# Kernel tuning notes

Measured on AMD Instinct MI355X. Metric: run time of the kernel, lower is better.

Reference implementation:

```python
import jax, jax.numpy as jnp
import numpy as np

M, NQ, NKV, DX, DT = 8, 1024, 1024, 512, 2
H, HD = 8, 64            # num_heads, head_dim
INNER = H * HD           # 512
KHID = 16                # kernel MLP hidden dim
SCALE = HD ** -0.5


def setup_inputs() -> dict:
    key = jax.random.key(0)
    ks = jax.random.split(key, 16)
    s = lambda fan_in: 1.0 / np.sqrt(fan_in)
    return {
        "xq": jax.random.normal(ks[0], (M, NQ, DX), jnp.float32),
        "xk": jax.random.normal(ks[1], (M, NKV, DX), jnp.float32),
        "xv": jax.random.normal(ks[2], (M, NKV, DX), jnp.float32),
        "tq": jax.random.normal(ks[3], (M, NQ, DT), jnp.float32),
        "tk": jax.random.normal(ks[4], (M, NKV, DT), jnp.float32),
        # attention projections (bias=False for q/k/v, Linear bias for out)
        "w_q": jax.random.normal(ks[5], (DX, INNER), jnp.float32) * s(DX),
        "w_k": jax.random.normal(ks[6], (DX, INNER), jnp.float32) * s(DX),
        "w_v": jax.random.normal(ks[7], (DX, INNER), jnp.float32) * s(DX),
        "w_out": jax.random.normal(ks[8], (INNER, DX), jnp.float32) * s(INNER),
        "b_out": jnp.zeros((DX,), jnp.float32),
        # kernel MLP: dt -> KHID -> H (per-head pairwise bias)
        "kw1": jax.random.normal(ks[9], (DT, KHID), jnp.float32) * s(DT),
        "kb1": jnp.zeros((KHID,), jnp.float32),
        "kw2": jax.random.normal(ks[10], (KHID, H), jnp.float32) * s(KHID),
        "kb2": jnp.zeros((H,), jnp.float32),
    }


def reference(xq, xk, xv, tq, tk, w_q, w_k, w_v, w_out, b_out, kw1, kb1, kw2, kb2):
    # pairwise differences of input locations: [m, nq, nkv, dt]
    diff = tq[:, :, None, :] - tk[:, None, :, :]
    # kernel MLP -> per-head bias, rearranged to [m, h, nq, nkv]
    hmid = jax.nn.relu(diff @ kw1 + kb1)          # [m, nq, nkv, KHID]
    dots = jnp.einsum('mqkc,ch->mhqk', hmid, kw2) + kb2[None, :, None, None]
    # token attention: standard scaled QK scores
    q = (xq @ w_q).reshape(M, NQ, H, HD)          # [m, nq, h, d]
    k = (xk @ w_k).reshape(M, NKV, H, HD)
    token_dots = jnp.einsum('mqhd,mkhd->mhqk', q, k) * SCALE
    dots = dots + token_dots
    attn = jax.nn.softmax(dots, axis=-1)          # softmax over keys
    v = (xv @ w_v).reshape(M, NKV, H, HD)
    out = jnp.einsum('mhqk,mkhd->mqhd', attn, v).reshape(M, NQ, INNER)
    return out @ w_out + b_out                    # [m, nq, dx]
```

## Files before the change

### kernel.cpp

```cpp
#include <hip/hip_runtime.h>


typedef unsigned short u16;
typedef unsigned int   u32;
typedef short bf8 __attribute__((ext_vector_type(8)));
typedef float f4  __attribute__((ext_vector_type(4)));
typedef _Float16 h2 __attribute__((ext_vector_type(2)));

#define Mb 8
#define LOG2E 1.44269504088896f
#define SCALE2 (0.125f * LOG2E)
#define NTOK 4194304

__device__ __forceinline__ u16 f2bf(float f) {
    union { float f; u32 u; } v; v.f = f;
    u32 r = v.u + 0x7fffu + ((v.u >> 16) & 1u);
    return (u16)(r >> 16);
}
__device__ __forceinline__ u32 pk2(float a, float b) {
    u32 r;
    asm("v_cvt_pk_bf16_f32 %0, %1, %2" : "=v"(r) : "v"(a), "v"(b));
    return r;
}
__device__ __forceinline__ void gl_lds16(const u16* g, u16* l) {
    __builtin_amdgcn_global_load_lds(
        (const __attribute__((address_space(1))) u32*)g,
        (__attribute__((address_space(3))) u32*)l, 16, 0, 0);
}
__device__ __forceinline__ h2 h2_of(u32 x) {
    union { u32 u; h2 h; } c; c.u = x; return c.h;
}
__device__ __forceinline__ u32 u_of(h2 x) {
    union { h2 h; u32 u; } c; c.h = x; return c.u;
}
__device__ __forceinline__ float dot2(h2 a, h2 b, float c) {
#if __has_builtin(__builtin_amdgcn_fdot2)
    return __builtin_amdgcn_fdot2(a, b, c, false);
#else
    return fmaf((float)a[0], (float)b[0], fmaf((float)a[1], (float)b[1], c));
#endif
}

struct PArgs {
    const float* ws[4];
    u16* dstW;
};

__global__ __launch_bounds__(256) void prep(PArgs p) {
    __shared__ u16 tl[64][80];
    const int tid = threadIdx.x;
    const int bb = blockIdx.x;
    const int mat = bb >> 6, t = bb & 63;
    const int kt = t >> 3, nt = t & 7;
    const float* src = p.ws[mat] + (size_t)kt * 64 * 512 + (size_t)nt * 64;
    const int r0 = tid >> 4, c4 = (tid & 15) * 4;
    #pragma unroll
    for (int rr = 0; rr < 4; ++rr) {
        const int row = r0 + rr * 16;
        float4 a = *(const float4*)(src + (size_t)row * 512 + c4);
        tl[c4 + 0][row] = f2bf(a.x);
        tl[c4 + 1][row] = f2bf(a.y);
        tl[c4 + 2][row] = f2bf(a.z);
        tl[c4 + 3][row] = f2bf(a.w);
    }
    __syncthreads();
    u16* dst = p.dstW + (size_t)mat * 262144 + (size_t)nt * 64 * 512 + (size_t)kt * 64;
    #pragma unroll
    for (int i = 0; i < 2; ++i) {
        const int s2 = tid + i * 256;
        const int nrow = s2 >> 3, k8 = (s2 & 7) * 8;
        *(uint4*)(dst + (size_t)nrow * 512 + k8) = *(const uint4*)&tl[nrow][k8];
    }
}

struct GArgs {
    const void*  A[3];
    const u16*   W[3];
    void*        C[3];
    const float* bias;
    int          modeT[3];
    int          outf32;
    int          af32;
};

__global__ __launch_bounds__(256) void gemm_mfma(GArgs g) {
    __shared__ u16 Xs[128][32];
    __shared__ u16 Ws[128][32];

    const int z   = blockIdx.z;
    const int tid = threadIdx.x;
    const int w = tid >> 6, lane = tid & 63, quad = lane >> 4, l16 = lane & 15;
    const int wm = w >> 1, wn = w & 1;
    const int n0 = blockIdx.x * 128, t0 = blockIdx.y * 128;
    const int trans = g.modeT[z];

    f4 acc[4][4];
    #pragma unroll
    for (int i = 0; i < 4; ++i)
        #pragma unroll
        for (int j = 0; j < 4; ++j) acc[i][j] = (f4)0.f;

    const int lrow  = lane >> 2;
    const int kslot = (lane & 3) ^ ((lane >> 3) & 3);
    u16* ldsW0 = &Ws[w * 32][0];
    u16* ldsW1 = &Ws[w * 32 + 16][0];
    const u16* gW0 = g.W[z] + (size_t)(n0 + w * 32 + lrow) * 512 + kslot * 8;
    const u16* gW1 = gW0 + 16 * 512;

    u16* ldsX0 = &Xs[w * 32][0];
    u16* ldsX1 = &Xs[w * 32 + 16][0];
    const u16* gA0 = (const u16*)g.A[z] + (size_t)(t0 + w * 32 + lrow) * 512 + kslot * 8;
    const u16* gA1 = gA0 + 16 * 512;
    const int arow_s = tid >> 1, ah = tid & 1;
    const float* aF = (const float*)g.A[z] + (size_t)(t0 + arow_s) * 512 + ah * 16;
    const int s_sw = (arow_s >> 1) & 3;
    u16* aw0 = &Xs[arow_s][((2 * ah)     ^ s_sw) * 8];
    u16* aw1 = &Xs[arow_s][((2 * ah + 1) ^ s_sw) * 8];

    const int rslot = (quad ^ ((l16 >> 1) & 3)) * 8;

    for (int kc = 0; kc < 512; kc += 32) {
        __syncthreads();
        if (g.af32) {
            float4 f0 = *(const float4*)(aF + kc);
            float4 f1 = *(const float4*)(aF + kc + 4);
            float4 f2 = *(const float4*)(aF + kc + 8);
            float4 f3 = *(const float4*)(aF + kc + 12);
            uint4 v0, v1;
            v0.x = pk2(f0.x, f0.y); v0.y = pk2(f0.z, f0.w);
            v0.z = pk2(f1.x, f1.y); v0.w = pk2(f1.z, f1.w);
            v1.x = pk2(f2.x, f2.y); v1.y = pk2(f2.z, f2.w);
            v1.z = pk2(f3.x, f3.y); v1.w = pk2(f3.z, f3.w);
            *(uint4*)aw0 = v0;
            *(uint4*)aw1 = v1;
        } else {
            gl_lds16(gA0 + kc, ldsX0);
            gl_lds16(gA1 + kc, ldsX1);
        }
        gl_lds16(gW0 + kc, ldsW0);
        gl_lds16(gW1 + kc, ldsW1);
        __syncthreads();

        const u16* Abase = trans ? &Xs[0][0] : &Ws[0][0];
        const u16* Bbase = trans ? &Ws[0][0] : &Xs[0][0];
        const int arow = (trans ? wm : wn) * 64;
        const int brow = (trans ? wn : wm) * 64;
        bf8 af[4], bf[4];
        #pragma unroll
        for (int i = 0; i < 4; ++i)
            af[i] = *(const bf8*)(Abase + (arow + i * 16 + l16) * 32 + rslot);
        #pragma unroll
        for (int j = 0; j < 4; ++j)
            bf[j] = *(const bf8*)(Bbase + (brow + j * 16 + l16) * 32 + rslot);
        #pragma unroll
        for (int i = 0; i < 4; ++i)
            #pragma unroll
            for (int j = 0; j < 4; ++j)
                acc[i][j] = __builtin_amdgcn_mfma_f32_16x16x32_bf16(af[i], bf[j], acc[i][j], 0, 0, 0);
    }

    if (g.outf32) {
        float* Co = (float*)g.C[z];
        #pragma unroll
        for (int i = 0; i < 4; ++i) {
            const int nb = n0 + wn * 64 + i * 16 + quad * 4;
            float4 bv = *(const float4*)&g.bias[nb];
            #pragma unroll
            for (int j = 0; j < 4; ++j) {
                const int tok = t0 + wm * 64 + j * 16 + l16;
                float4 st;
                st.x = acc[i][j][0] + bv.x; st.y = acc[i][j][1] + bv.y;
                st.z = acc[i][j][2] + bv.z; st.w = acc[i][j][3] + bv.w;
                *(float4*)&Co[(size_t)tok * 512 + nb] = st;
            }
        }
    } else if (!trans) {
        u16* C = (u16*)g.C[z];
        #pragma unroll
        for (int i = 0; i < 4; ++i) {
            const int nb = n0 + wn * 64 + i * 16 + quad * 4;
            #pragma unroll
            for (int j = 0; j < 4; ++j) {
                const int tok = t0 + wm * 64 + j * 16 + l16;
                uint2 pw;
                pw.x = pk2(acc[i][j][0], acc[i][j][1]);
                pw.y = pk2(acc[i][j][2], acc[i][j][3]);
                *(uint2*)&C[(size_t)tok * 512 + nb] = pw;
            }
        }
    } else {
        u16* Vt = (u16*)g.C[z];
        #pragma unroll
        for (int i = 0; i < 4; ++i) {
            const int tokb = t0 + wm * 64 + i * 16 + quad * 4;
            const int mb = tokb >> 10, tb = tokb & 1023;
            #pragma unroll
            for (int j = 0; j < 4; ++j) {
                const int n = n0 + wn * 64 + j * 16 + l16;
                uint2 pw;
                pw.x = pk2(acc[i][j][0], acc[i][j][1]);
                pw.y = pk2(acc[i][j][2], acc[i][j][3]);
                *(uint2*)&Vt[(size_t)mb * 524288 + (size_t)n * 1024 + tb] = pw;
            }
        }
    }
}

__global__ __launch_bounds__(512) void attn_mfma(
    const u16* __restrict__ Q, const u16* __restrict__ K,
    const u16* __restrict__ Vt,
    const float* __restrict__ tqp, const float* __restrict__ tkp,
    const float* __restrict__ kw1, const float* __restrict__ kb1,
    const float* __restrict__ kw2,
    u16* __restrict__ O)
{
    __shared__ u16 sK[2][8][64][8];
    __shared__ u16 sV[2][8][64][8];
    __shared__ u32 sv2[2][8][68];
    __shared__ u16 sP[8][16][68];

    const int tid = threadIdx.x;
    const int w = tid >> 6, lane = tid & 63, quad = lane >> 4, l16 = lane & 15;
    const int b = (blockIdx.z * 8 + blockIdx.y) * 8 + blockIdx.x;
    const int xc = b & 7, j = b >> 3;
    const int hm = xc * 8 + (j & 7);
    const int qt = j >> 3;
    const int h = hm & 7, m = hm >> 3;
    const int q0 = qt * 128;
    const size_t qtok = (size_t)m * 1024 + q0 + w * 16 + l16;

    bf8 qf[2];
    {
        const u16* qp = Q + qtok * 512 + h * 64 + quad * 8;
        qf[0] = *(const bf8*)qp;
        qf[1] = *(const bf8*)(qp + 32);
    }
    h2 u2[8], w2p[8];
    {
        const float t0v = tqp[qtok * 2], t1v = tqp[qtok * 2 + 1];
        #pragma unroll
        for (int cp = 0; cp < 8; ++cp) {
            const int c0 = 2 * cp, c1 = 2 * cp + 1;
            float ua = fmaf(t0v, kw1[c0], fmaf(t1v, kw1[16 + c0], kb1[c0]));
            float ub = fmaf(t0v, kw1[c1], fmaf(t1v, kw1[16 + c1], kb1[c1]));
            u2[cp][0]  = (_Float16)ua;  u2[cp][1]  = (_Float16)ub;
            w2p[cp][0] = (_Float16)(LOG2E * kw2[c0 * 8 + h]);
            w2p[cp][1] = (_Float16)(LOG2E * kw2[c1 * 8 + h]);
        }
    }
    const float w0a = kw1[2 * w],     w1a = kw1[16 + 2 * w];
    const float w0b = kw1[2 * w + 1], w1b = kw1[16 + 2 * w + 1];

    const u16* gK = K + ((size_t)m * 1024 + lane) * 512 + h * 64 + w * 8;
    const u16* gV = Vt + (size_t)m * 524288 + (size_t)(h * 64 + lane) * 1024 + w * 8;
    const float* gT = tkp + (size_t)m * 2048 + lane * 2;

    float mrun = -1e30f, lrun = 0.f;
    f4 o[4];
    #pragma unroll
    for (int d = 0; d < 4; ++d) o[d] = (f4)0.f;

    auto STAGE = [&](int kt2, int nb) {
        const int k0n = kt2 * 64;
        float2 t = *(const float2*)(gT + k0n * 2);
        h2 pv;
        pv[0] = (_Float16)fmaf(t.x, w0a, t.y * w1a);
        pv[1] = (_Float16)fmaf(t.x, w0b, t.y * w1b);
        sv2[nb][w][lane] = u_of(pv);
        gl_lds16(gK + (size_t)k0n * 512, &sK[nb][w][0][0]);
        gl_lds16(gV + k0n,               &sV[nb][w][0][0]);
    };

    STAGE(0, 0);
    __syncthreads();

    int cur = 0;
    for (int kt = 0; kt < 16; ++kt) {
        if (kt < 15) STAGE(kt + 1, cur ^ 1);

        f4 s[4];
        #pragma unroll
        for (int msub = 0; msub < 4; ++msub) {
            bf8 kf0 = *(const bf8*)&sK[cur][quad][msub * 16 + l16][0];
            bf8 kf1 = *(const bf8*)&sK[cur][4 + quad][msub * 16 + l16][0];
            s[msub] = __builtin_amdgcn_mfma_f32_16x16x32_bf16(kf0, qf[0], (f4)0.f, 0, 0, 0);
            s[msub] = __builtin_amdgcn_mfma_f32_16x16x32_bf16(kf1, qf[1], s[msub], 0, 0, 0);
        }
        #pragma unroll
        for (int msub = 0; msub < 4; ++msub) {
            const int kb = msub * 16 + quad * 4;
            f4 b2 = (f4)0.f;
            #pragma unroll
            for (int cp = 0; cp < 8; ++cp) {
                uint4 vv = *(const uint4*)&sv2[cur][cp][kb];
                const h2 uc = u2[cp], wc = w2p[cp];
                const h2 z = (h2)(_Float16)0.f;
                h2 d0 = uc - h2_of(vv.x);
                h2 d1 = uc - h2_of(vv.y);
                h2 d2 = uc - h2_of(vv.z);
                h2 d3 = uc - h2_of(vv.w);
                d0 = __builtin_elementwise_max(d0, z);
                d1 = __builtin_elementwise_max(d1, z);
                d2 = __builtin_elementwise_max(d2, z);
                d3 = __builtin_elementwise_max(d3, z);
                b2[0] = dot2(d0, wc, b2[0]);
                b2[1] = dot2(d1, wc, b2[1]);
                b2[2] = dot2(d2, wc, b2[2]);
                b2[3] = dot2(d3, wc, b2[3]);
            }
            s[msub] = s[msub] * SCALE2 + b2;
        }
        float mx = -1e30f;
        #pragma unroll
        for (int msub = 0; msub < 4; ++msub) {
            mx = fmaxf(mx, fmaxf(fmaxf(s[msub][0], s[msub][1]),
                                 fmaxf(s[msub][2], s[msub][3])));
        }
        mx = fmaxf(mx, __shfl_xor(mx, 16));
        mx = fmaxf(mx, __shfl_xor(mx, 32));
        const float mnew = fmaxf(mrun, mx);
        float ps = 0.f;
        #pragma unroll
        for (int msub = 0; msub < 4; ++msub) {
            #pragma unroll
            for (int r = 0; r < 4; ++r) {
                float p = exp2f(s[msub][r] - mnew);
                s[msub][r] = p;
                ps += p;
            }
        }
        ps += __shfl_xor(ps, 16);
        ps += __shfl_xor(ps, 32);
        if (__all(mx <= mrun)) {
            lrun += ps;
        } else {
            const float alpha = exp2f(mrun - mnew);
            lrun = lrun * alpha + ps;
            mrun = mnew;
            #pragma unroll
            for (int d = 0; d < 4; ++d) o[d] = o[d] * alpha;
        }
        #pragma unroll
        for (int msub = 0; msub < 4; ++msub) {
            uint2 pw;
            pw.x = pk2(s[msub][0], s[msub][1]);
            pw.y = pk2(s[msub][2], s[msub][3]);
            *(uint2*)&sP[w][l16][msub * 16 + quad * 4] = pw;
        }
        #pragma unroll
        for (int dsub = 0; dsub < 4; ++dsub) {
            #pragma unroll
            for (int kc2 = 0; kc2 < 2; ++kc2) {
                bf8 vf = *(const bf8*)&sV[cur][kc2 * 4 + quad][dsub * 16 + l16][0];
                bf8 pf = *(const bf8*)&sP[w][l16][kc2 * 32 + quad * 8];
                o[dsub] = __builtin_amdgcn_mfma_f32_16x16x32_bf16(vf, pf, o[dsub], 0, 0, 0);
            }
        }

        if (kt < 15) __syncthreads();
        cur ^= 1;
    }

    const float inv = 1.f / lrun;
    #pragma unroll
    for (int dsub = 0; dsub < 4; ++dsub) {
        uint2 pw;
        pw.x = pk2(o[dsub][0] * inv, o[dsub][1] * inv);
        pw.y = pk2(o[dsub][2] * inv, o[dsub][3] * inv);
        *(uint2*)&O[qtok * 512 + h * 64 + dsub * 16 + quad * 4] = pw;
    }
}

extern "C" void kernel_launch(void* const* d_in, const int* in_sizes, int n_in,
                              void* d_out, int out_size, void* d_ws, size_t ws_size,
                              hipStream_t stream) {
    const float* xq    = (const float*)d_in[0];
    const float* xk    = (const float*)d_in[1];
    const float* xv    = (const float*)d_in[2];
    const float* tq    = (const float*)d_in[3];
    const float* tk    = (const float*)d_in[4];
    const float* w_q   = (const float*)d_in[5];
    const float* w_k   = (const float*)d_in[6];
    const float* w_v   = (const float*)d_in[7];
    const float* w_out = (const float*)d_in[8];
    const float* b_out = (const float*)d_in[9];
    const float* kw1   = (const float*)d_in[10];
    const float* kb1   = (const float*)d_in[11];
    const float* kw2   = (const float*)d_in[12];

    u16* Q  = (u16*)d_ws;
    u16* Kp = Q  + NTOK;
    u16* Vt = Kp + NTOK;
    u16* O  = Vt + NTOK;
    u16* Wq = O  + 3 * (size_t)NTOK;
    u16* Wk = Wq + 262144;
    u16* Wv = Wk + 262144;
    u16* Wo = Wv + 262144;

    PArgs p;
    p.ws[0] = w_q; p.ws[1] = w_k; p.ws[2] = w_v; p.ws[3] = w_out;
    p.dstW = Wq;
    prep<<<dim3(256), 256, 0, stream>>>(p);

    GArgs gq;
    gq.A[0] = xq;  gq.A[1] = xk;  gq.A[2] = xv;
    gq.W[0] = Wq;  gq.W[1] = Wk;  gq.W[2] = Wv;
    gq.C[0] = Q;   gq.C[1] = Kp;  gq.C[2] = Vt;
    gq.bias = nullptr;
    gq.modeT[0] = 0; gq.modeT[1] = 0; gq.modeT[2] = 1;
    gq.outf32 = 0; gq.af32 = 1;
    gemm_mfma<<<dim3(4, 64, 3), 256, 0, stream>>>(gq);

    attn_mfma<<<dim3(8, 8, Mb), 512, 0, stream>>>(Q, Kp, Vt, tq, tk,
                                                  kw1, kb1, kw2, O);

    GArgs go;
    go.A[0] = O;   go.A[1] = O;   go.A[2] = O;
    go.W[0] = Wo;  go.W[1] = Wo;  go.W[2] = Wo;
    go.C[0] = d_out; go.C[1] = d_out; go.C[2] = d_out;
    go.bias = b_out;
    go.modeT[0] = 0; go.modeT[1] = 0; go.modeT[2] = 0;
    go.outf32 = 1; go.af32 = 0;
    gemm_mfma<<<dim3(4, 64, 1), 256, 0, stream>>>(go);
}
```

Measured before the change: 259.7 us.

## Fuse output projection into attention epilogue via per-head atomic accumulation

Removes the separate output-projection GEMM and its bf16 O intermediate. Each attention wave now multiplies its normalized head output by the matching slice of W_out with MFMA and atomically adds the partial result into the fp32 output. The prep kernel pre-fills the output with the bias, and the gemm kernel drops its unused fp32-output and bf16-A paths. It trades a kernel launch and an O round-trip for many scattered, non-coalesced float atomics (eight heads per output element). It also replaces exp2 with the LOG2E folded into the weights by __expf, which adds a multiply per element.

After: 616.0 us. +137.2%, slower.

```diff
diff --git a/kernel.cpp b/kernel.cpp
--- a/kernel.cpp
+++ b/kernel.cpp
@@ -8,8 +8,7 @@
 typedef _Float16 h2 __attribute__((ext_vector_type(2)));
 
 #define Mb 8
-#define LOG2E 1.44269504088896f
-#define SCALE2 (0.125f * LOG2E)
+#define SCALE 0.125f
 #define NTOK 4194304
 
 __device__ __forceinline__ u16 f2bf(float f) {
@@ -44,32 +43,45 @@
 struct PArgs {
     const float* ws[4];
     u16* dstW;
+    const float* bias;
+    float* outp;
 };
 
 __global__ __launch_bounds__(256) void prep(PArgs p) {
     __shared__ u16 tl[64][80];
     const int tid = threadIdx.x;
-    const int bb = blockIdx.x;
-    const int mat = bb >> 6, t = bb & 63;
-    const int kt = t >> 3, nt = t & 7;
-    const float* src = p.ws[mat] + (size_t)kt * 64 * 512 + (size_t)nt * 64;
-    const int r0 = tid >> 4, c4 = (tid & 15) * 4;
-    #pragma unroll
-    for (int rr = 0; rr < 4; ++rr) {
-        const int row = r0 + rr * 16;
-        float4 a = *(const float4*)(src + (size_t)row * 512 + c4);
-        tl[c4 + 0][row] = f2bf(a.x);
-        tl[c4 + 1][row] = f2bf(a.y);
-        tl[c4 + 2][row] = f2bf(a.z);
-        tl[c4 + 3][row] = f2bf(a.w);
-    }
-    __syncthreads();
-    u16* dst = p.dstW + (size_t)mat * 262144 + (size_t)nt * 64 * 512 + (size_t)kt * 64;
-    #pragma unroll
-    for (int i = 0; i < 2; ++i) {
-        const int s2 = tid + i * 256;
-        const int nrow = s2 >> 3, k8 = (s2 & 7) * 8;
-        *(uint4*)(dst + (size_t)nrow * 512 + k8) = *(const uint4*)&tl[nrow][k8];
+    const int b = blockIdx.x;
+    if (b < 256) {
+        const int mat = b >> 6, t = b & 63;
+        const int kt = t >> 3, nt = t & 7;
+        const float* src = p.ws[mat] + (size_t)kt * 64 * 512 + (size_t)nt * 64;
+        const int r0 = tid >> 4, c4 = (tid & 15) * 4;
+        #pragma unroll
+        for (int rr = 0; rr < 4; ++rr) {
+            const int row = r0 + rr * 16;
+            float4 a = *(const float4*)(src + (size_t)row * 512 + c4);
+            tl[c4 + 0][row] = f2bf(a.x);
+            tl[c4 + 1][row] = f2bf(a.y);
+            tl[c4 + 2][row] = f2bf(a.z);
+            tl[c4 + 3][row] = f2bf(a.w);
+        }
+        __syncthreads();
+        u16* dst = p.dstW + (size_t)mat * 262144 + (size_t)nt * 64 * 512 + (size_t)kt * 64;
+        #pragma unroll
+        for (int i = 0; i < 2; ++i) {
+            const int s2 = tid + i * 256;
+            const int nrow = s2 >> 3, k8 = (s2 & 7) * 8;
+            *(uint4*)(dst + (size_t)nrow * 512 + k8) = *(const uint4*)&tl[nrow][k8];
+        }
+    } else {
+        const int bb = b - 256;
+        const int tok = bb * 16 + (tid >> 4);
+        const int c0 = (tid & 15) * 8;
+        float* dst = p.outp + (size_t)tok * 512;
+        const float4* bsrc = (const float4*)p.bias;
+        #pragma unroll
+        for (int i = 0; i < 8; ++i)
+            *(float4*)(dst + (c0 + i) * 4) = bsrc[c0 + i];
     }
 }
 
@@ -77,10 +89,7 @@
     const void*  A[3];
     const u16*   W[3];
     void*        C[3];
-    const float* bias;
     int          modeT[3];
-    int          outf32;
-    int          af32;
 };
 
 __global__ __launch_bounds__(256) void gemm_mfma(GArgs g) {
@@ -107,10 +116,6 @@
     const u16* gW0 = g.W[z] + (size_t)(n0 + w * 32 + lrow) * 512 + kslot * 8;
     const u16* gW1 = gW0 + 16 * 512;
 
-    u16* ldsX0 = &Xs[w * 32][0];
-    u16* ldsX1 = &Xs[w * 32 + 16][0];
-    const u16* gA0 = (const u16*)g.A[z] + (size_t)(t0 + w * 32 + lrow) * 512 + kslot * 8;
-    const u16* gA1 = gA0 + 16 * 512;
     const int arow_s = tid >> 1, ah = tid & 1;
     const float* aF = (const float*)g.A[z] + (size_t)(t0 + arow_s) * 512 + ah * 16;
     const int s_sw = (arow_s >> 1) & 3;
@@ -121,7 +126,7 @@
 
     for (int kc = 0; kc < 512; kc += 32) {
         __syncthreads();
-        if (g.af32) {
+        {
             float4 f0 = *(const float4*)(aF + kc);
             float4 f1 = *(const float4*)(aF + kc + 4);
             float4 f2 = *(const float4*)(aF + kc + 8);
@@ -133,9 +138,6 @@
             v1.z = pk2(f3.x, f3.y); v1.w = pk2(f3.z, f3.w);
             *(uint4*)aw0 = v0;
             *(uint4*)aw1 = v1;
-        } else {
-            gl_lds16(gA0 + kc, ldsX0);
-            gl_lds16(gA1 + kc, ldsX1);
         }
         gl_lds16(gW0 + kc, ldsW0);
         gl_lds16(gW1 + kc, ldsW1);
@@ -159,22 +161,7 @@
                 acc[i][j] = __builtin_amdgcn_mfma_f32_16x16x32_bf16(af[i], bf[j], acc[i][j], 0, 0, 0);
     }
 
-    if (g.outf32) {
-        float* Co = (float*)g.C[z];
-        #pragma unroll
-        for (int i = 0; i < 4; ++i) {
-            const int nb = n0 + wn * 64 + i * 16 + quad * 4;
-            float4 bv = *(const float4*)&g.bias[nb];
-            #pragma unroll
-            for (int j = 0; j < 4; ++j) {
-                const int tok = t0 + wm * 64 + j * 16 + l16;
-                float4 st;
-                st.x = acc[i][j][0] + bv.x; st.y = acc[i][j][1] + bv.y;
-                st.z = acc[i][j][2] + bv.z; st.w = acc[i][j][3] + bv.w;
-                *(float4*)&Co[(size_t)tok * 512 + nb] = st;
-            }
-        }
-    } else if (!trans) {
+    if (!trans) {
         u16* C = (u16*)g.C[z];
         #pragma unroll
         for (int i = 0; i < 4; ++i) {
@@ -212,7 +199,7 @@
     const float* __restrict__ tqp, const float* __restrict__ tkp,
     const float* __restrict__ kw1, const float* __restrict__ kb1,
     const float* __restrict__ kw2,
-    u16* __restrict__ O)
+    const u16* __restrict__ Wo, float* __restrict__ Oout)
 {
     __shared__ u16 sK[2][8][64][8];
     __shared__ u16 sV[2][8][64][8];
@@ -243,9 +230,8 @@
             const int c0 = 2 * cp, c1 = 2 * cp + 1;
             float ua = fmaf(t0v, kw1[c0], fmaf(t1v, kw1[16 + c0], kb1[c0]));
             float ub = fmaf(t0v, kw1[c1], fmaf(t1v, kw1[16 + c1], kb1[c1]));
-            u2[cp][0]  = (_Float16)ua;  u2[cp][1]  = (_Float16)ub;
-            w2p[cp][0] = (_Float16)(LOG2E * kw2[c0 * 8 + h]);
-            w2p[cp][1] = (_Float16)(LOG2E * kw2[c1 * 8 + h]);
+            u2[cp][0]  = (_Float16)ua;              u2[cp][1]  = (_Float16)ub;
+            w2p[cp][0] = (_Float16)kw2[c0 * 8 + h]; w2p[cp][1] = (_Float16)kw2[c1 * 8 + h];
         }
     }
     const float w0a = kw1[2 * w],     w1a = kw1[16 + 2 * w];
@@ -308,7 +294,7 @@
                 b2[2] = dot2(d2, wc, b2[2]);
                 b2[3] = dot2(d3, wc, b2[3]);
             }
-            s[msub] = s[msub] * SCALE2 + b2;
+            s[msub] = s[msub] * SCALE + b2;
         }
         float mx = -1e30f;
         #pragma unroll
@@ -324,7 +310,7 @@
         for (int msub = 0; msub < 4; ++msub) {
             #pragma unroll
             for (int r = 0; r < 4; ++r) {
-                float p = exp2f(s[msub][r] - mnew);
+                float p = __expf(s[msub][r] - mnew);
                 s[msub][r] = p;
                 ps += p;
             }
@@ -334,7 +320,7 @@
         if (__all(mx <= mrun)) {
             lrun += ps;
         } else {
-            const float alpha = exp2f(mrun - mnew);
+            const float alpha = __expf(mrun - mnew);
             lrun = lrun * alpha + ps;
             mrun = mnew;
             #pragma unroll
@@ -367,7 +353,23 @@
         uint2 pw;
         pw.x = pk2(o[dsub][0] * inv, o[dsub][1] * inv);
         pw.y = pk2(o[dsub][2] * inv, o[dsub][3] * inv);
-        *(uint2*)&O[qtok * 512 + h * 64 + dsub * 16 + quad * 4] = pw;
+        *(uint2*)&sP[w][l16][dsub * 16 + quad * 4] = pw;
+    }
+    bf8 of0 = *(const bf8*)&sP[w][l16][quad * 8];
+    bf8 of1 = *(const bf8*)&sP[w][l16][32 + quad * 8];
+    float* outp = Oout + qtok * 512;
+    const u16* woA = Wo + (size_t)l16 * 512 + h * 64 + quad * 8;
+    #pragma unroll 4
+    for (int nf = 0; nf < 32; ++nf) {
+        const u16* wp = woA + (size_t)nf * 16 * 512;
+        bf8 af0 = *(const bf8*)wp;
+        bf8 af1 = *(const bf8*)(wp + 32);
+        f4 a = __builtin_amdgcn_mfma_f32_16x16x32_bf16(af0, of0, (f4)0.f, 0, 0, 0);
+        a = __builtin_amdgcn_mfma_f32_16x16x32_bf16(af1, of1, a, 0, 0, 0);
+        const int nb = nf * 16 + quad * 4;
+        #pragma unroll
+        for (int r = 0; r < 4; ++r)
+            unsafeAtomicAdd(&outp[nb + r], a[r]);
     }
 }
 
@@ -391,8 +393,7 @@
     u16* Q  = (u16*)d_ws;
     u16* Kp = Q  + NTOK;
     u16* Vt = Kp + NTOK;
-    u16* O  = Vt + NTOK;
-    u16* Wq = O  + 3 * (size_t)NTOK;
+    u16* Wq = Vt + NTOK;
     u16* Wk = Wq + 262144;
     u16* Wv = Wk + 262144;
     u16* Wo = Wv + 262144;
@@ -400,26 +401,18 @@
     PArgs p;
     p.ws[0] = w_q; p.ws[1] = w_k; p.ws[2] = w_v; p.ws[3] = w_out;
     p.dstW = Wq;
-    prep<<<dim3(256), 256, 0, stream>>>(p);
+    p.bias = b_out;
+    p.outp = (float*)d_out;
+    prep<<<dim3(768), 256, 0, stream>>>(p);
 
     GArgs gq;
     gq.A[0] = xq;  gq.A[1] = xk;  gq.A[2] = xv;
     gq.W[0] = Wq;  gq.W[1] = Wk;  gq.W[2] = Wv;
     gq.C[0] = Q;   gq.C[1] = Kp;  gq.C[2] = Vt;
-    gq.bias = nullptr;
     gq.modeT[0] = 0; gq.modeT[1] = 0; gq.modeT[2] = 1;
-    gq.outf32 = 0; gq.af32 = 1;
     gemm_mfma<<<dim3(4, 64, 3), 256, 0, stream>>>(gq);
 
     attn_mfma<<<dim3(8, 8, Mb), 512, 0, stream>>>(Q, Kp, Vt, tq, tk,
-                                                  kw1, kb1, kw2, O);
-
-    GArgs go;
-    go.A[0] = O;   go.A[1] = O;   go.A[2] = O;
-    go.W[0] = Wo;  go.W[1] = Wo;  go.W[2] = Wo;
-    go.C[0] = d_out; go.C[1] = d_out; go.C[2] = d_out;
-    go.bias = b_out;
-    go.modeT[0] = 0; go.modeT[1] = 0; go.modeT[2] = 0;
-    go.outf32 = 1; go.af32 = 0;
-    gemm_mfma<<<dim3(4, 64, 1), 256, 0, stream>>>(go);
-}
+                                                  kw1, kb1, kw2,
+                                                  Wo, (float*)d_out);
+}
```
